# Optimization experiments

Measured on AMD Instinct MI355X. Metric: run time of the kernel, lower is better.

Reference implementation:

```python
import jax, jax.numpy as jnp
import numpy as np

N_NODES = 50000
N_EDGES = 800000
N_GRAPHS = 64


def graph_conv(x, edge_index, w_rel, b_rel, w_root):
    # PyG GraphConv with aggr='add':
    #   out = lin_rel(sum_{j in N(i)} x_j) + lin_root(x_i)
    src, dst = edge_index[0], edge_index[1]
    agg = jax.ops.segment_sum(x[src], dst, num_segments=x.shape[0])  # [N, d_in]
    return agg @ w_rel + b_rel + x @ w_root  # [N, d_out]


def scatter_mean(x, batch, num_segments):
    s = jax.ops.segment_sum(x, batch, num_segments=num_segments)
    cnt = jax.ops.segment_sum(jnp.ones((x.shape[0],), x.dtype), batch,
                              num_segments=num_segments)
    return s / jnp.maximum(cnt, 1.0)[:, None]


def setup_inputs() -> dict:
    key = jax.random.key(0)
    ks = jax.random.split(key, 8)
    d_feat, d_hid, d_out = 128, 128, 128
    x = jax.random.normal(ks[0], (N_NODES, d_feat), dtype=jnp.float32)
    edge_index = jax.random.randint(ks[1], (2, N_EDGES), 0, N_NODES, dtype=jnp.int64)
    batch = jnp.sort(jax.random.randint(ks[2], (N_NODES,), 0, N_GRAPHS, dtype=jnp.int64))

    def glorot(k, shape):
        fan_in = shape[0]
        return jax.random.normal(k, shape, dtype=jnp.float32) / np.sqrt(fan_in)

    return {
        "x": x,
        "edge_index": edge_index,
        "batch": batch,
        "w_rel1": glorot(ks[3], (d_feat, d_hid)),
        "b_rel1": jnp.zeros((d_hid,), jnp.float32),
        "w_root1": glorot(ks[4], (d_feat, d_hid)),
        "w_rel2": glorot(ks[5], (d_hid, 2 * d_hid)),
        "b_rel2": jnp.zeros((2 * d_hid,), jnp.float32),
        "w_root2": glorot(ks[6], (d_hid, 2 * d_hid)),
        "w_rel3": glorot(ks[7], (2 * d_hid, d_out)),
        "b_rel3": jnp.zeros((d_out,), jnp.float32),
        "w_root3": glorot(jax.random.fold_in(key, 99), (2 * d_hid, d_out)),
    }


def reference(x, edge_index, batch,
              w_rel1, b_rel1, w_root1,
              w_rel2, b_rel2, w_root2,
              w_rel3, b_rel3, w_root3):
    h = jax.nn.elu(graph_conv(x, edge_index, w_rel1, b_rel1, w_root1))
    h = jax.nn.elu(graph_conv(h, edge_index, w_rel2, b_rel2, w_root2))
    h = jax.nn.elu(graph_conv(h, edge_index, w_rel3, b_rel3, w_root3))
    return scatter_mean(h, batch, N_GRAPHS)  # [num_graphs, n_out]
```

## Files before the change

### kernel.cpp

```cpp
#include <hip/hip_runtime.h>
#include <math.h>

#define NN 50000
#define NE 800000
#define NG 64
#define NBK 196
#define ECH 4082
#define TOTH (NBK * NBK)
#define NBH 151

typedef __attribute__((ext_vector_type(8))) __bf16 bf16x8;
typedef __attribute__((ext_vector_type(8))) short short8;
typedef __attribute__((ext_vector_type(4))) float f32x4;

__device__ inline unsigned short f2bf(float f) {
    unsigned int u = __float_as_uint(f);
    u += 0x7fffu + ((u >> 16) & 1u);
    return (unsigned short)(u >> 16);
}
__device__ inline float bflo(unsigned int v) { return __uint_as_float(v << 16); }
__device__ inline float bfhi(unsigned int v) { return __uint_as_float(v & 0xffff0000u); }

__global__ __launch_bounds__(256) void cvt_k(const float* __restrict__ in,
                                             unsigned short* __restrict__ outp) {
    int i = blockIdx.x * 256 + threadIdx.x;
    if (i < NN * 32) {
        float4 v = ((const float4*)in)[i];
        unsigned int p0 = ((unsigned int)f2bf(v.y) << 16) | f2bf(v.x);
        unsigned int p1 = ((unsigned int)f2bf(v.w) << 16) | f2bf(v.z);
        ((uint2*)outp)[i] = make_uint2(p0, p1);
    }
}

__global__ __launch_bounds__(256) void hist_k(const int* __restrict__ dst,
                                              int* __restrict__ H) {
    __shared__ int h[NBK];
    int t = threadIdx.x, k = blockIdx.x;
    if (t < NBK) h[t] = 0;
    __syncthreads();
    int e0 = k * ECH, e1 = min(NE, e0 + ECH);
    for (int e = e0 + t; e < e1; e += 256) atomicAdd(&h[dst[e] >> 8], 1);
    __syncthreads();
    if (t < NBK) H[t * NBK + k] = h[t];
}

__global__ __launch_bounds__(256) void hsum_k(const int* __restrict__ H,
                                              int* __restrict__ hb) {
    int i = blockIdx.x * 256 + threadIdx.x;
    int v = (i < TOTH) ? H[i] : 0;
    for (int off = 32; off; off >>= 1) v += __shfl_xor(v, off, 64);
    __shared__ int ws[4];
    if ((threadIdx.x & 63) == 0) ws[threadIdx.x >> 6] = v;
    __syncthreads();
    if (threadIdx.x == 0) hb[blockIdx.x] = ws[0] + ws[1] + ws[2] + ws[3];
}

__global__ __launch_bounds__(256) void hscan_k(const int* __restrict__ hb,
                                               int* __restrict__ hoff) {
    __shared__ int s[256];
    int t = threadIdx.x;
    int v = (t < NBH) ? hb[t] : 0;
    s[t] = v; __syncthreads();
    for (int off = 1; off < 256; off <<= 1) {
        int u = (t >= off) ? s[t - off] : 0;
        __syncthreads(); s[t] += u; __syncthreads();
    }
    hoff[t] = (t == 0) ? 0 : s[t - 1];
}

__global__ __launch_bounds__(256) void happly_k(const int* __restrict__ H,
                                                const int* __restrict__ hoff,
                                                int* __restrict__ S) {
    int t = threadIdx.x;
    int i = blockIdx.x * 256 + t;
    int v = (i < TOTH) ? H[i] : 0;
    __shared__ int s[256];
    s[t] = v; __syncthreads();
    for (int off = 1; off < 256; off <<= 1) {
        int u = (t >= off) ? s[t - off] : 0;
        __syncthreads(); s[t] += u; __syncthreads();
    }
    if (i < TOTH) S[i] = hoff[blockIdx.x] + s[t] - v;
}

__global__ __launch_bounds__(256) void scatter_k(const int* __restrict__ src,
                                                 const int* __restrict__ dst,
                                                 const int* __restrict__ S,
                                                 int* __restrict__ tmp) {
    __shared__ int cur[NBK];
    int t = threadIdx.x, k = blockIdx.x;
    if (t < NBK) cur[t] = S[t * NBK + k];
    __syncthreads();
    int e0 = k * ECH, e1 = min(NE, e0 + ECH);
    for (int e = e0 + t; e < e1; e += 256) {
        int d = dst[e];
        int p = atomicAdd(&cur[d >> 8], 1);
        tmp[p] = ((d & 255) << 16) | src[e];
    }
}

__global__ __launch_bounds__(256) void csr_k(const int* __restrict__ tmp,
                                             const int* __restrict__ S,
                                             int* __restrict__ rowptr,
                                             int* __restrict__ colsrc) {
    __shared__ int hist[256], off[256], cur[256];
    int t = threadIdx.x, b = blockIdx.x;
    int base = S[b * NBK];
    int next = (b < NBK - 1) ? S[(b + 1) * NBK] : NE;
    int cntb = next - base;
    hist[t] = 0;
    __syncthreads();
    for (int i = t; i < cntb; i += 256) atomicAdd(&hist[tmp[base + i] >> 16], 1);
    __syncthreads();
    int v = hist[t];
    off[t] = v; __syncthreads();
    for (int o = 1; o < 256; o <<= 1) {
        int u = (t >= o) ? off[t - o] : 0;
        __syncthreads(); off[t] += u; __syncthreads();
    }
    int excl = off[t] - v;
    int node = b * 256 + t;
    if (node <= NN) rowptr[node] = base + excl;
    cur[t] = excl;
    __syncthreads();
    for (int i = t; i < cntb; i += 256) {
        int e = tmp[base + i];
        int p = atomicAdd(&cur[e >> 16], 1);
        colsrc[base + p] = e & 0xffff;
    }
}

__global__ __launch_bounds__(256) void aggb_k(const unsigned short* __restrict__ feat,
                                              const int* __restrict__ rowptr,
                                              const int* __restrict__ colsrc,
                                              unsigned short* __restrict__ outp) {
    int node = __builtin_amdgcn_readfirstlane((int)(blockIdx.x * 4 + (threadIdx.x >> 6)));
    int lane = threadIdx.x & 63;
    int beg = rowptr[node], end = rowptr[node + 1];
    float ax = 0.f, ay = 0.f;
    int e = beg;
    for (; e + 2 <= end; e += 2) {
        int s0 = colsrc[e], s1 = colsrc[e + 1];
        unsigned int v0 = *(const unsigned int*)&feat[(size_t)s0 * 128 + lane * 2];
        unsigned int v1 = *(const unsigned int*)&feat[(size_t)s1 * 128 + lane * 2];
        ax += bflo(v0); ay += bfhi(v0);
        ax += bflo(v1); ay += bfhi(v1);
    }
    if (e < end) {
        unsigned int v0 = *(const unsigned int*)&feat[(size_t)colsrc[e] * 128 + lane * 2];
        ax += bflo(v0); ay += bfhi(v0);
    }
    unsigned int p = ((unsigned int)f2bf(ay) << 16) | f2bf(ax);
    *(unsigned int*)&outp[(size_t)node * 128 + lane * 2] = p;
}

template <int KA, int N, bool TWO, bool BIAS, bool ELU, bool SPLIT>
__global__ __launch_bounds__(256) void gemm_k(const unsigned short* __restrict__ A1,
                                              const unsigned short* __restrict__ A2,
                                              const float* __restrict__ W1,
                                              const float* __restrict__ W2,
                                              const float* __restrict__ bias,
                                              unsigned short* __restrict__ Cout,
                                              unsigned short* __restrict__ Cout2) {
    constexpr int KTOT = TWO ? 2 * KA : KA;
    __shared__ __attribute__((aligned(16))) unsigned short As[64][40];
    __shared__ __attribute__((aligned(16))) unsigned short Bs[64][40];
    const int t = threadIdx.x;
    const int m0 = blockIdx.x * 64;
    const int n0 = blockIdx.y * 64;
    const int wv = t >> 6, lane = t & 63, qd = lane >> 4, l16 = lane & 15;
    f32x4 acc[4] = {};

    const int arow = t >> 2;
    const int akk  = (t & 3) << 3;
    const int wkl  = t >> 3;
    const int wng  = (t & 7) << 3;
    const int gm = m0 + arow;

    for (int k0 = 0; k0 < KTOT; k0 += 32) {
        {
            int kabs = k0 + akk;
            const unsigned short* src = (TWO && kabs >= KA)
                ? (A2 + (size_t)gm * KA + (kabs - KA))
                : (A1 + (size_t)gm * KA + kabs);
            short8 sv = {};
            if (gm < NN) sv = *(const short8*)src;
            *(short8*)&As[arow][akk] = sv;
        }
        {
            int kabs = k0 + wkl;
            const float* src;
            if (SPLIT) {
                const float* wsel = (n0 < 128) ? W1 : W2;
                src = wsel + (size_t)kabs * 128 + ((n0 + wng) & 127);
            } else if (TWO && kabs >= KA) {
                src = W2 + (size_t)(kabs - KA) * N + n0 + wng;
            } else {
                src = W1 + (size_t)kabs * N + n0 + wng;
            }
            float4 v0 = *(const float4*)src;
            float4 v1 = *(const float4*)(src + 4);
            Bs[wng + 0][wkl] = f2bf(v0.x); Bs[wng + 1][wkl] = f2bf(v0.y);
            Bs[wng + 2][wkl] = f2bf(v0.z); Bs[wng + 3][wkl] = f2bf(v0.w);
            Bs[wng + 4][wkl] = f2bf(v1.x); Bs[wng + 5][wkl] = f2bf(v1.y);
            Bs[wng + 6][wkl] = f2bf(v1.z); Bs[wng + 7][wkl] = f2bf(v1.w);
        }
        __syncthreads();
        bf16x8 af = *(const bf16x8*)&As[wv * 16 + l16][qd * 8];
#pragma unroll
        for (int j = 0; j < 4; ++j) {
            bf16x8 bfv = *(const bf16x8*)&Bs[j * 16 + l16][qd * 8];
            acc[j] = __builtin_amdgcn_mfma_f32_16x16x32_bf16(af, bfv, acc[j], 0, 0, 0);
        }
        __syncthreads();
    }
#pragma unroll
    for (int j = 0; j < 4; ++j) {
#pragma unroll
        for (int r = 0; r < 4; ++r) {
            int mm = m0 + wv * 16 + qd * 4 + r;
            if (mm < NN) {
                int nn = n0 + j * 16 + l16;
                float v = acc[j][r];
                if (BIAS) v += bias[nn];
                if (ELU) v = v > 0.f ? v : (__expf(v) - 1.f);
                unsigned short b = f2bf(v);
                if (SPLIT) {
                    unsigned short* dst = (nn < 128) ? Cout : Cout2;
                    dst[(size_t)mm * 128 + (nn & 127)] = b;
                } else {
                    Cout[(size_t)mm * N + nn] = b;
                }
            }
        }
    }
}

__global__ void bounds_k(const int* __restrict__ batch, int* __restrict__ bounds) {
    int g = threadIdx.x;
    if (g > NG) return;
    int lo = 0, hi = NN;
    while (lo < hi) {
        int mid = (lo + hi) >> 1;
        if (batch[mid] < g) lo = mid + 1; else hi = mid;
    }
    bounds[g] = lo;
}

__global__ __launch_bounds__(128) void finalize2_k(const unsigned short* __restrict__ aggy,
                                                   const unsigned short* __restrict__ rr,
                                                   const float* __restrict__ b3,
                                                   const int* __restrict__ batch,
                                                   float* __restrict__ outsum) {
    const int CH = 25;
    int n0 = blockIdx.x * CH;
    int c = threadIdx.x;
    float bias = b3[c];
    int g = batch[n0];
    float acc = 0.f;
    for (int i = 0; i < CH; ++i) {
        int n = n0 + i;
        int gn = batch[n];
        if (gn != g) {
            unsafeAtomicAdd(&outsum[(size_t)g * 128 + c], acc);
            acc = 0.f; g = gn;
        }
        size_t idx = (size_t)n * 128 + c;
        float v = __uint_as_float((unsigned int)aggy[idx] << 16)
                + __uint_as_float((unsigned int)rr[idx] << 16) + bias;
        v = v > 0.f ? v : (__expf(v) - 1.f);
        acc += v;
    }
    unsafeAtomicAdd(&outsum[(size_t)g * 128 + c], acc);
}

__global__ void divide_k(const int* __restrict__ bounds, float* __restrict__ out) {
    int i = blockIdx.x * 256 + threadIdx.x;
    if (i < NG * 128) {
        int g = i >> 7;
        float c = (float)(bounds[g + 1] - bounds[g]);
        out[i] /= fmaxf(c, 1.f);
    }
}

extern "C" void kernel_launch(void* const* d_in, const int* in_sizes, int n_in,
                              void* d_out, int out_size, void* d_ws, size_t ws_size,
                              hipStream_t stream) {
    const float* x       = (const float*)d_in[0];
    const int*   ei      = (const int*)d_in[1];
    const int*   batch   = (const int*)d_in[2];
    const float* w_rel1  = (const float*)d_in[3];
    const float* b_rel1  = (const float*)d_in[4];
    const float* w_root1 = (const float*)d_in[5];
    const float* w_rel2  = (const float*)d_in[6];
    const float* b_rel2  = (const float*)d_in[7];
    const float* w_root2 = (const float*)d_in[8];
    const float* w_rel3  = (const float*)d_in[9];
    const float* b_rel3  = (const float*)d_in[10];
    const float* w_root3 = (const float*)d_in[11];
    const int* esrc = ei;
    const int* edst = ei + NE;

    unsigned short* Ab = (unsigned short*)d_ws;
    unsigned short* Bb = Ab + (size_t)NN * 128;
    unsigned short* Cb = Bb + (size_t)NN * 128;
    unsigned short* xb = Cb + (size_t)NN * 256;
    int* rowptr = (int*)(xb + (size_t)NN * 128);
    int* colsrc = rowptr + (NN + 1);
    int* tmp    = colsrc + NE;
    int* H      = tmp + NE;
    int* S      = H + TOTH;
    int* hb     = S + TOTH;
    int* hoff   = hb + 256;
    int* bounds = hoff + 256;
    float* outp = (float*)d_out;

    cvt_k<<<(NN * 32 + 255) / 256, 256, 0, stream>>>(x, xb);
    hist_k<<<NBK, 256, 0, stream>>>(edst, H);
    hsum_k<<<NBH, 256, 0, stream>>>(H, hb);
    hscan_k<<<1, 256, 0, stream>>>(hb, hoff);
    happly_k<<<NBH, 256, 0, stream>>>(H, hoff, S);
    scatter_k<<<NBK, 256, 0, stream>>>(esrc, edst, S, tmp);
    csr_k<<<NBK, 256, 0, stream>>>(tmp, S, rowptr, colsrc);

    dim3 g2(782, 2), g4(782, 4);

    aggb_k<<<NN / 4, 256, 0, stream>>>(xb, rowptr, colsrc, Ab);
    gemm_k<128, 128, true, true, true, false><<<g2, 256, 0, stream>>>(Ab, xb, w_rel1, w_root1, b_rel1, Bb, nullptr);

    aggb_k<<<NN / 4, 256, 0, stream>>>(Bb, rowptr, colsrc, Ab);
    gemm_k<128, 256, true, true, true, false><<<g4, 256, 0, stream>>>(Ab, Bb, w_rel2, w_root2, b_rel2, Cb, nullptr);

    gemm_k<256, 256, false, false, false, true><<<g4, 256, 0, stream>>>(Cb, nullptr, w_rel3, w_root3, nullptr, Ab, Bb);
    aggb_k<<<NN / 4, 256, 0, stream>>>(Ab, rowptr, colsrc, Cb);

    hipMemsetAsync(outp, 0, NG * 128 * sizeof(float), stream);
    bounds_k<<<1, 128, 0, stream>>>(batch, bounds);
    finalize2_k<<<NN / 25, 128, 0, stream>>>(Cb, Bb, b_rel3, batch, outp);
    divide_k<<<(NG * 128 + 255) / 256, 256, 0, stream>>>(bounds, outp);
}
```

Measured before the change: 361.9 us.

## Pre-transpose weights to bf16 and use 128x128 GEMM tiles with direct-to-LDS loads

Adds a kernel that converts and transposes all three layer weights to bf16 once per call, so the GEMM no longer converts fp32 weights per tile. The GEMM tile grows from 64x64 to 128x128, with each wave computing a 64x64 sub-tile of 16 MFMAs per k-step. Operands are staged into LDS with global_load_lds instructions. Buffers are padded to a multiple of 128 rows so the unguarded loads stay in bounds. The risks are higher register pressure from the 4x4 accumulator array and fewer blocks (391 or 782), which lowers occupancy and parallelism.

```diff
diff --git a/kernel.cpp b/kernel.cpp
--- a/kernel.cpp
+++ b/kernel.cpp
@@ -2,6 +2,7 @@
 #include <math.h>
 
 #define NN 50000
+#define NNP 50048
 #define NE 800000
 #define NG 64
 #define NBK 196
@@ -20,6 +21,11 @@
 }
 __device__ inline float bflo(unsigned int v) { return __uint_as_float(v << 16); }
 __device__ inline float bfhi(unsigned int v) { return __uint_as_float(v & 0xffff0000u); }
+
+#define GLD_LDS16(g, l)                                                          \
+    __builtin_amdgcn_global_load_lds(                                            \
+        (const __attribute__((address_space(1))) unsigned int*)(g),              \
+        (__attribute__((address_space(3))) unsigned int*)(l), 16, 0, 0)
 
 __global__ __launch_bounds__(256) void cvt_k(const float* __restrict__ in,
                                              unsigned short* __restrict__ outp) {
@@ -29,6 +35,31 @@
         unsigned int p0 = ((unsigned int)f2bf(v.y) << 16) | f2bf(v.x);
         unsigned int p1 = ((unsigned int)f2bf(v.w) << 16) | f2bf(v.z);
         ((uint2*)outp)[i] = make_uint2(p0, p1);
+    }
+}
+
+__global__ __launch_bounds__(256) void wt_k(const float* __restrict__ wr1,
+                                            const float* __restrict__ wo1,
+                                            const float* __restrict__ wr2,
+                                            const float* __restrict__ wo2,
+                                            const float* __restrict__ wr3,
+                                            const float* __restrict__ wo3,
+                                            unsigned short* __restrict__ W1T,
+                                            unsigned short* __restrict__ W2T,
+                                            unsigned short* __restrict__ W3T) {
+    int id = blockIdx.x * 256 + threadIdx.x;
+    if (id < 32768) {
+        int n = id >> 8, k = id & 255;
+        float v = (k < 128) ? wr1[k * 128 + n] : wo1[(k - 128) * 128 + n];
+        W1T[id] = f2bf(v);
+    } else if (id < 98304) {
+        int j = id - 32768; int n = j >> 8, k = j & 255;
+        float v = (k < 128) ? wr2[k * 256 + n] : wo2[(k - 128) * 256 + n];
+        W2T[j] = f2bf(v);
+    } else if (id < 163840) {
+        int j = id - 98304; int n = j >> 8, k = j & 255;
+        float v = (n < 128) ? wr3[k * 128 + n] : wo3[k * 128 + (n - 128)];
+        W3T[j] = f2bf(v);
     }
 }
 
@@ -157,79 +188,74 @@
 template <int KA, int N, bool TWO, bool BIAS, bool ELU, bool SPLIT>
 __global__ __launch_bounds__(256) void gemm_k(const unsigned short* __restrict__ A1,
                                               const unsigned short* __restrict__ A2,
-                                              const float* __restrict__ W1,
-                                              const float* __restrict__ W2,
+                                              const unsigned short* __restrict__ WT,
                                               const float* __restrict__ bias,
                                               unsigned short* __restrict__ Cout,
                                               unsigned short* __restrict__ Cout2) {
     constexpr int KTOT = TWO ? 2 * KA : KA;
-    __shared__ __attribute__((aligned(16))) unsigned short As[64][40];
-    __shared__ __attribute__((aligned(16))) unsigned short Bs[64][40];
+    __shared__ __attribute__((aligned(16))) unsigned short As[128 * 32];
+    __shared__ __attribute__((aligned(16))) unsigned short Bs[128 * 32];
     const int t = threadIdx.x;
-    const int m0 = blockIdx.x * 64;
-    const int n0 = blockIdx.y * 64;
-    const int wv = t >> 6, lane = t & 63, qd = lane >> 4, l16 = lane & 15;
-    f32x4 acc[4] = {};
-
-    const int arow = t >> 2;
-    const int akk  = (t & 3) << 3;
-    const int wkl  = t >> 3;
-    const int wng  = (t & 7) << 3;
-    const int gm = m0 + arow;
+    const int wv = t >> 6, lane = t & 63;
+    const int qd = lane >> 4, l16 = lane & 15;
+    const int m0 = blockIdx.x * 128, n0 = blockIdx.y * 128;
+    const int mh = (wv & 1) * 64, nh = (wv >> 1) * 64;
+    const int srow = lane >> 2;
+    const int skk  = (lane & 3) * 8;
+
+    f32x4 acc[4][4] = {};
 
     for (int k0 = 0; k0 < KTOT; k0 += 32) {
-        {
-            int kabs = k0 + akk;
-            const unsigned short* src = (TWO && kabs >= KA)
-                ? (A2 + (size_t)gm * KA + (kabs - KA))
-                : (A1 + (size_t)gm * KA + kabs);
-            short8 sv = {};
-            if (gm < NN) sv = *(const short8*)src;
-            *(short8*)&As[arow][akk] = sv;
+        const unsigned short* Abase = (TWO && k0 >= KA) ? (A2 + (k0 - KA)) : (A1 + k0);
+#pragma unroll
+        for (int i = 0; i < 2; ++i) {
+            int chunk = wv * 2 + i;
+            const unsigned short* g = Abase + (size_t)(m0 + chunk * 16 + srow) * KA + skk;
+            GLD_LDS16(g, &As[chunk * 512]);
         }
-        {
-            int kabs = k0 + wkl;
-            const float* src;
-            if (SPLIT) {
-                const float* wsel = (n0 < 128) ? W1 : W2;
-                src = wsel + (size_t)kabs * 128 + ((n0 + wng) & 127);
-            } else if (TWO && kabs >= KA) {
-                src = W2 + (size_t)(kabs - KA) * N + n0 + wng;
-            } else {
-                src = W1 + (size_t)kabs * N + n0 + wng;
-            }
-            float4 v0 = *(const float4*)src;
-            float4 v1 = *(const float4*)(src + 4);
-            Bs[wng + 0][wkl] = f2bf(v0.x); Bs[wng + 1][wkl] = f2bf(v0.y);
-            Bs[wng + 2][wkl] = f2bf(v0.z); Bs[wng + 3][wkl] = f2bf(v0.w);
-            Bs[wng + 4][wkl] = f2bf(v1.x); Bs[wng + 5][wkl] = f2bf(v1.y);
-            Bs[wng + 6][wkl] = f2bf(v1.z); Bs[wng + 7][wkl] = f2bf(v1.w);
+        const unsigned short* Wbase = WT + k0;
+#pragma unroll
+        for (int i = 0; i < 2; ++i) {
+            int chunk = wv * 2 + i;
+            const unsigned short* g = Wbase + (size_t)(n0 + chunk * 16 + srow) * KTOT + skk;
+            GLD_LDS16(g, &Bs[chunk * 512]);
         }
         __syncthreads();
-        bf16x8 af = *(const bf16x8*)&As[wv * 16 + l16][qd * 8];
-#pragma unroll
-        for (int j = 0; j < 4; ++j) {
-            bf16x8 bfv = *(const bf16x8*)&Bs[j * 16 + l16][qd * 8];
-            acc[j] = __builtin_amdgcn_mfma_f32_16x16x32_bf16(af, bfv, acc[j], 0, 0, 0);
-        }
+        bf16x8 af[4], bfr[4];
+#pragma unroll
+        for (int mi = 0; mi < 4; ++mi)
+            af[mi] = *(const bf16x8*)&As[(mh + mi * 16 + l16) * 32 + qd * 8];
+#pragma unroll
+        for (int ni = 0; ni < 4; ++ni)
+            bfr[ni] = *(const bf16x8*)&Bs[(nh + ni * 16 + l16) * 32 + qd * 8];
+#pragma unroll
+        for (int mi = 0; mi < 4; ++mi)
+#pragma unroll
+            for (int ni = 0; ni < 4; ++ni)
+                acc[mi][ni] = __builtin_amdgcn_mfma_f32_16x16x32_bf16(
+                    af[mi], bfr[ni], acc[mi][ni], 0, 0, 0);
         __syncthreads();
     }
-#pragma unroll
-    for (int j = 0; j < 4; ++j) {
-#pragma unroll
-        for (int r = 0; r < 4; ++r) {
-            int mm = m0 + wv * 16 + qd * 4 + r;
-            if (mm < NN) {
-                int nn = n0 + j * 16 + l16;
-                float v = acc[j][r];
-                if (BIAS) v += bias[nn];
-                if (ELU) v = v > 0.f ? v : (__expf(v) - 1.f);
-                unsigned short b = f2bf(v);
-                if (SPLIT) {
-                    unsigned short* dst = (nn < 128) ? Cout : Cout2;
-                    dst[(size_t)mm * 128 + (nn & 127)] = b;
-                } else {
-                    Cout[(size_t)mm * N + nn] = b;
+
+#pragma unroll
+    for (int mi = 0; mi < 4; ++mi) {
+#pragma unroll
+        for (int ni = 0; ni < 4; ++ni) {
+#pragma unroll
+            for (int r = 0; r < 4; ++r) {
+                int mm = m0 + mh + mi * 16 + qd * 4 + r;
+                if (mm < NN) {
+                    int nn = n0 + nh + ni * 16 + l16;
+                    float v = acc[mi][ni][r];
+                    if (BIAS) v += bias[nn];
+                    if (ELU) v = v > 0.f ? v : (__expf(v) - 1.f);
+                    unsigned short b = f2bf(v);
+                    if (SPLIT) {
+                        unsigned short* dst = (nn < 128) ? Cout : Cout2;
+                        dst[(size_t)mm * 128 + (nn & 127)] = b;
+                    } else {
+                        Cout[(size_t)mm * N + nn] = b;
+                    }
                 }
             }
         }
@@ -302,10 +328,13 @@
     const int* edst = ei + NE;
 
     unsigned short* Ab = (unsigned short*)d_ws;
-    unsigned short* Bb = Ab + (size_t)NN * 128;
-    unsigned short* Cb = Bb + (size_t)NN * 128;
-    unsigned short* xb = Cb + (size_t)NN * 256;
-    int* rowptr = (int*)(xb + (size_t)NN * 128);
+    unsigned short* Bb = Ab + (size_t)NNP * 128;
+    unsigned short* Cb = Bb + (size_t)NNP * 128;
+    unsigned short* xb = Cb + (size_t)NNP * 256;
+    unsigned short* W1T = xb + (size_t)NNP * 128;
+    unsigned short* W2T = W1T + 128 * 256;
+    unsigned short* W3T = W2T + 256 * 256;
+    int* rowptr = (int*)(W3T + 256 * 256);
     int* colsrc = rowptr + (NN + 1);
     int* tmp    = colsrc + NE;
     int* H      = tmp + NE;
@@ -316,6 +345,8 @@
     float* outp = (float*)d_out;
 
     cvt_k<<<(NN * 32 + 255) / 256, 256, 0, stream>>>(x, xb);
+    wt_k<<<640, 256, 0, stream>>>(w_rel1, w_root1, w_rel2, w_root2, w_rel3, w_root3,
+                                  W1T, W2T, W3T);
     hist_k<<<NBK, 256, 0, stream>>>(edst, H);
     hsum_k<<<NBH, 256, 0, stream>>>(H, hb);
     hscan_k<<<1, 256, 0, stream>>>(hb, hoff);
@@ -323,15 +354,15 @@
     scatter_k<<<NBK, 256, 0, stream>>>(esrc, edst, S, tmp);
     csr_k<<<NBK, 256, 0, stream>>>(tmp, S, rowptr, colsrc);
 
-    dim3 g2(782, 2), g4(782, 4);
+    dim3 g1(NNP / 128, 1), g2(NNP / 128, 2);
 
     aggb_k<<<NN / 4, 256, 0, stream>>>(xb, rowptr, colsrc, Ab);
-    gemm_k<128, 128, true, true, true, false><<<g2, 256, 0, stream>>>(Ab, xb, w_rel1, w_root1, b_rel1, Bb, nullptr);
+    gemm_k<128, 128, true, true, true, false><<<g1, 256, 0, stream>>>(Ab, xb, W1T, b_rel1, Bb, nullptr);
 
     aggb_k<<<NN / 4, 256, 0, stream>>>(Bb, rowptr, colsrc, Ab);
-    gemm_k<128, 256, true, true, true, false><<<g4, 256, 0, stream>>>(Ab, Bb, w_rel2, w_root2, b_rel2, Cb, nullptr);
-
-    gemm_k<256, 256, false, false, false, true><<<g4, 256, 0, stream>>>(Cb, nullptr, w_rel3, w_root3, nullptr, Ab, Bb);
+    gemm_k<128, 256, true, true, true, false><<<g2, 256, 0, stream>>>(Ab, Bb, W2T, b_rel2, Cb, nullptr);
+
+    gemm_k<256, 256, false, false, false, true><<<g2, 256, 0, stream>>>(Cb, nullptr, W3T, nullptr, Ab, Bb);
     aggb_k<<<NN / 4, 256, 0, stream>>>(Ab, rowptr, colsrc, Cb);
 
     hipMemsetAsync(outp, 0, NG * 128 * sizeof(float), stream);
```

New measurement: 335.0 us. 7.4% less time.
